# Kernel optimization log

Hardware: AMD Instinct MI355X
Metric: run time of the kernel (lower is better)

Reference implementation:

```python
import jax, jax.numpy as jnp
import numpy as np

N, D, B = 500000, 256, 2048

def setup_inputs() -> dict:
    key = jax.random.key(0)
    k1, k2, k3 = jax.random.split(key, 3)
    x = jax.random.normal(k1, (N, D), dtype=jnp.float32)
    batch_id = jnp.sort(jax.random.randint(k2, (N,), 0, B, dtype=jnp.int64))
    gate_w = jax.random.normal(k3, (D, 1), dtype=jnp.float32) * (1.0 / np.sqrt(D))
    gate_b = jnp.zeros((1,), dtype=jnp.float32)
    return {"x": x, "batch_id": batch_id, "batch_size": B, "gate_w": gate_w, "gate_b": gate_b}

def reference(x, batch_id, batch_size, gate_w, gate_b):
    # gate: Linear(D,1) + Sigmoid -> (N, 1)
    weights = jax.nn.sigmoid(x @ gate_w + gate_b)  # (N, 1)
    weighted = x * weights                          # (N, D)
    # scatter_add by graph id -> (B, D)
    pooled = jax.ops.segment_sum(weighted, batch_id, num_segments=batch_size)
    return pooled
```

## Files before the change

### kernel.cpp

```cpp
#include <hip/hip_runtime.h>

#define D_DIM 256
#define NWAVES 8192

typedef float v4f __attribute__((ext_vector_type(4)));

__device__ __forceinline__ float dot4(v4f v, v4f w) {
    return v[0]*w[0] + v[1]*w[1] + v[2]*w[2] + v[3]*w[3];
}
__device__ __forceinline__ float sigmoidf_(float t) {
    return 1.0f / (1.0f + __expf(-t));
}
__device__ __forceinline__ v4f vzero() {
    v4f z = {0.f, 0.f, 0.f, 0.f};
    return z;
}
__device__ __forceinline__ void flush_acc(float* __restrict__ out, int b,
                                          int lane, v4f acc) {
    float* p = out + (size_t)b * D_DIM + lane * 4;
    unsafeAtomicAdd(p + 0, acc[0]);
    unsafeAtomicAdd(p + 1, acc[1]);
    unsafeAtomicAdd(p + 2, acc[2]);
    unsafeAtomicAdd(p + 3, acc[3]);
}

__global__ __launch_bounds__(256) void attentive_readout_kernel(
    const float* __restrict__ x,
    const int* __restrict__ bid,
    const float* __restrict__ gw,
    const float* __restrict__ gb,
    float* __restrict__ out,
    int n)
{
    int gtid = blockIdx.x * blockDim.x + threadIdx.x;
    int wave = gtid >> 6;
    int lane = threadIdx.x & 63;

    const int base = n / NWAVES, rem = n % NWAVES;
    long long r0 = (long long)wave * base + (wave < rem ? wave : rem);
    long long r1 = r0 + base + (wave < rem ? 1 : 0);

    const v4f w4 = *(const v4f*)(gw + lane * 4);
    const float bias = gb[0];

    v4f acc = vzero();
    int cur = bid[r0];

    const float* px = x + (size_t)r0 * D_DIM + lane * 4;
    long long r = r0;
    const int nfull = (int)((r1 - r0) >> 2);

    v4f c0, c1, c2, c3;
    int cb0, cb1, cb2, cb3;
    if (nfull > 0) {
        c0 = __builtin_nontemporal_load((const v4f*)(px + 0 * D_DIM));
        c1 = __builtin_nontemporal_load((const v4f*)(px + 1 * D_DIM));
        c2 = __builtin_nontemporal_load((const v4f*)(px + 2 * D_DIM));
        c3 = __builtin_nontemporal_load((const v4f*)(px + 3 * D_DIM));
        cb0 = bid[r + 0]; cb1 = bid[r + 1]; cb2 = bid[r + 2]; cb3 = bid[r + 3];
    }

    for (int it = 0; it < nfull; ++it) {
        v4f n0, n1, n2, n3;
        int nb0 = 0, nb1 = 0, nb2 = 0, nb3 = 0;
        const float* pn = px + 4 * D_DIM;
        const bool more = (it + 1 < nfull);
        if (more) {
            n0 = __builtin_nontemporal_load((const v4f*)(pn + 0 * D_DIM));
            n1 = __builtin_nontemporal_load((const v4f*)(pn + 1 * D_DIM));
            n2 = __builtin_nontemporal_load((const v4f*)(pn + 2 * D_DIM));
            n3 = __builtin_nontemporal_load((const v4f*)(pn + 3 * D_DIM));
            nb0 = bid[r + 4]; nb1 = bid[r + 5]; nb2 = bid[r + 6]; nb3 = bid[r + 7];
        } else {
            n0 = c0; n1 = c1; n2 = c2; n3 = c3;
        }

        float s0 = dot4(c0, w4);
        float s1 = dot4(c1, w4);
        float s2 = dot4(c2, w4);
        float s3 = dot4(c3, w4);
        #pragma unroll
        for (int off = 32; off > 0; off >>= 1) {
            s0 += __shfl_xor(s0, off, 64);
            s1 += __shfl_xor(s1, off, 64);
            s2 += __shfl_xor(s2, off, 64);
            s3 += __shfl_xor(s3, off, 64);
        }
        float g0 = sigmoidf_(s0 + bias);
        float g1 = sigmoidf_(s1 + bias);
        float g2 = sigmoidf_(s2 + bias);
        float g3 = sigmoidf_(s3 + bias);

        if ((cb0 == cur) & (cb1 == cur) & (cb2 == cur) & (cb3 == cur)) {
            acc += c0 * g0 + c1 * g1 + c2 * g2 + c3 * g3;
        } else {
            if (cb0 != cur) { flush_acc(out, cur, lane, acc); acc = vzero(); cur = cb0; }
            acc += c0 * g0;
            if (cb1 != cur) { flush_acc(out, cur, lane, acc); acc = vzero(); cur = cb1; }
            acc += c1 * g1;
            if (cb2 != cur) { flush_acc(out, cur, lane, acc); acc = vzero(); cur = cb2; }
            acc += c2 * g2;
            if (cb3 != cur) { flush_acc(out, cur, lane, acc); acc = vzero(); cur = cb3; }
            acc += c3 * g3;
        }

        c0 = n0; c1 = n1; c2 = n2; c3 = n3;
        cb0 = nb0; cb1 = nb1; cb2 = nb2; cb3 = nb3;
        px = pn; r += 4;
    }

    for (; r < r1; ++r) {
        v4f v = __builtin_nontemporal_load((const v4f*)px);
        px += D_DIM;
        float s = dot4(v, w4);
        #pragma unroll
        for (int off = 32; off > 0; off >>= 1)
            s += __shfl_xor(s, off, 64);
        float g = sigmoidf_(s + bias);
        int b = bid[r];
        if (b != cur) { flush_acc(out, cur, lane, acc); acc = vzero(); cur = b; }
        acc += v * g;
    }
    flush_acc(out, cur, lane, acc);
}

extern "C" void kernel_launch(void* const* d_in, const int* in_sizes, int n_in,
                              void* d_out, int out_size, void* d_ws, size_t ws_size,
                              hipStream_t stream) {
    const float* x   = (const float*)d_in[0];
    const int*   bid = (const int*)d_in[1];
    const float* gw  = (const float*)d_in[3];
    const float* gb  = (const float*)d_in[4];
    float*       out = (float*)d_out;

    const int n = in_sizes[0] / D_DIM;

    hipMemsetAsync(d_out, 0, (size_t)out_size * sizeof(float), stream);

    const int threads = 256;
    const int blocks  = NWAVES / 4;

    attentive_readout_kernel<<<blocks, threads, 0, stream>>>(
        x, bid, gw, gb, out, n);
}
```

Baseline: 106.7 us.

## Double-buffer row groups per wave and use fixed 64-row wave chunks

The streaming loop now keeps two 4-row groups in flight in a ping-pong register scheme, so 8 rows of loads are outstanding while one group is reduced and accumulated. The work split changes from 8192 waves with uneven row ranges to fixed aligned 64-row chunks per wave, which lets the batch ids be fetched with a single int4 load. The aim is more memory-level parallelism on a bandwidth-bound stream. The cost is more live vector registers, which can lower occupancy.

```diff
diff --git a/kernel.cpp b/kernel.cpp
--- a/kernel.cpp
+++ b/kernel.cpp
@@ -1,7 +1,7 @@
 #include <hip/hip_runtime.h>
 
 #define D_DIM 256
-#define NWAVES 8192
+#define RPW   64
 
 typedef float v4f __attribute__((ext_vector_type(4)));
 
@@ -24,6 +24,53 @@
     unsafeAtomicAdd(p + 3, acc[3]);
 }
 
+__device__ __forceinline__ void prefetch_group(v4f& c0, v4f& c1, v4f& c2, v4f& c3,
+                                               int4& cb,
+                                               const float* px, const int* pb,
+                                               bool pred) {
+    if (pred) {
+        c0 = __builtin_nontemporal_load((const v4f*)(px + 0 * D_DIM));
+        c1 = __builtin_nontemporal_load((const v4f*)(px + 1 * D_DIM));
+        c2 = __builtin_nontemporal_load((const v4f*)(px + 2 * D_DIM));
+        c3 = __builtin_nontemporal_load((const v4f*)(px + 3 * D_DIM));
+        cb = *(const int4*)pb;
+    }
+}
+
+__device__ __forceinline__ void process_group(v4f c0, v4f c1, v4f c2, v4f c3,
+                                              int4 cb, v4f w4, float bias,
+                                              v4f& acc, int& cur,
+                                              float* __restrict__ out, int lane) {
+    float s0 = dot4(c0, w4);
+    float s1 = dot4(c1, w4);
+    float s2 = dot4(c2, w4);
+    float s3 = dot4(c3, w4);
+    #pragma unroll
+    for (int off = 32; off > 0; off >>= 1) {
+        s0 += __shfl_xor(s0, off, 64);
+        s1 += __shfl_xor(s1, off, 64);
+        s2 += __shfl_xor(s2, off, 64);
+        s3 += __shfl_xor(s3, off, 64);
+    }
+    float g0 = sigmoidf_(s0 + bias);
+    float g1 = sigmoidf_(s1 + bias);
+    float g2 = sigmoidf_(s2 + bias);
+    float g3 = sigmoidf_(s3 + bias);
+
+    if ((cb.x == cur) & (cb.y == cur) & (cb.z == cur) & (cb.w == cur)) {
+        acc += c0 * g0 + c1 * g1 + c2 * g2 + c3 * g3;
+    } else {
+        if (cb.x != cur) { flush_acc(out, cur, lane, acc); acc = vzero(); cur = cb.x; }
+        acc += c0 * g0;
+        if (cb.y != cur) { flush_acc(out, cur, lane, acc); acc = vzero(); cur = cb.y; }
+        acc += c1 * g1;
+        if (cb.z != cur) { flush_acc(out, cur, lane, acc); acc = vzero(); cur = cb.z; }
+        acc += c2 * g2;
+        if (cb.w != cur) { flush_acc(out, cur, lane, acc); acc = vzero(); cur = cb.w; }
+        acc += c3 * g3;
+    }
+}
+
 __global__ __launch_bounds__(256) void attentive_readout_kernel(
     const float* __restrict__ x,
     const int* __restrict__ bid,
@@ -36,9 +83,11 @@
     int wave = gtid >> 6;
     int lane = threadIdx.x & 63;
 
-    const int base = n / NWAVES, rem = n % NWAVES;
-    long long r0 = (long long)wave * base + (wave < rem ? wave : rem);
-    long long r1 = r0 + base + (wave < rem ? 1 : 0);
+    long long r0 = (long long)wave * RPW;
+    if (r0 >= n) return;
+    long long r1 = r0 + RPW;
+    if (r1 > n) r1 = n;
+    const int ngroups = (int)((r1 - r0) >> 2);
 
     const v4f w4 = *(const v4f*)(gw + lane * 4);
     const float bias = gb[0];
@@ -46,69 +95,34 @@
     v4f acc = vzero();
     int cur = bid[r0];
 
-    const float* px = x + (size_t)r0 * D_DIM + lane * 4;
-    long long r = r0;
-    const int nfull = (int)((r1 - r0) >> 2);
+    const float* pxa = x + (size_t)r0 * D_DIM + lane * 4;
+    const float* pxb = pxa + 4 * D_DIM;
+    const int*   pba = bid + r0;
+    const int*   pbb = pba + 4;
 
-    v4f c0, c1, c2, c3;
-    int cb0, cb1, cb2, cb3;
-    if (nfull > 0) {
-        c0 = __builtin_nontemporal_load((const v4f*)(px + 0 * D_DIM));
-        c1 = __builtin_nontemporal_load((const v4f*)(px + 1 * D_DIM));
-        c2 = __builtin_nontemporal_load((const v4f*)(px + 2 * D_DIM));
-        c3 = __builtin_nontemporal_load((const v4f*)(px + 3 * D_DIM));
-        cb0 = bid[r + 0]; cb1 = bid[r + 1]; cb2 = bid[r + 2]; cb3 = bid[r + 3];
+    v4f a0, a1, a2, a3, b0, b1, b2, b3;
+    int4 ab, bb;
+    prefetch_group(a0, a1, a2, a3, ab, pxa, pba, ngroups > 0);
+    prefetch_group(b0, b1, b2, b3, bb, pxb, pbb, ngroups > 1);
+
+    int g = 0;
+    for (; g + 2 <= ngroups; g += 2) {
+        process_group(a0, a1, a2, a3, ab, w4, bias, acc, cur, out, lane);
+        prefetch_group(a0, a1, a2, a3, ab, pxa + 8 * D_DIM, pba + 8,
+                       g + 2 < ngroups);
+        pxa += 8 * D_DIM; pba += 8;
+
+        process_group(b0, b1, b2, b3, bb, w4, bias, acc, cur, out, lane);
+        prefetch_group(b0, b1, b2, b3, bb, pxb + 8 * D_DIM, pbb + 8,
+                       g + 3 < ngroups);
+        pxb += 8 * D_DIM; pbb += 8;
+    }
+    if (g < ngroups) {
+        process_group(a0, a1, a2, a3, ab, w4, bias, acc, cur, out, lane);
     }
 
-    for (int it = 0; it < nfull; ++it) {
-        v4f n0, n1, n2, n3;
-        int nb0 = 0, nb1 = 0, nb2 = 0, nb3 = 0;
-        const float* pn = px + 4 * D_DIM;
-        const bool more = (it + 1 < nfull);
-        if (more) {
-            n0 = __builtin_nontemporal_load((const v4f*)(pn + 0 * D_DIM));
-            n1 = __builtin_nontemporal_load((const v4f*)(pn + 1 * D_DIM));
-            n2 = __builtin_nontemporal_load((const v4f*)(pn + 2 * D_DIM));
-            n3 = __builtin_nontemporal_load((const v4f*)(pn + 3 * D_DIM));
-            nb0 = bid[r + 4]; nb1 = bid[r + 5]; nb2 = bid[r + 6]; nb3 = bid[r + 7];
-        } else {
-            n0 = c0; n1 = c1; n2 = c2; n3 = c3;
-        }
-
-        float s0 = dot4(c0, w4);
-        float s1 = dot4(c1, w4);
-        float s2 = dot4(c2, w4);
-        float s3 = dot4(c3, w4);
-        #pragma unroll
-        for (int off = 32; off > 0; off >>= 1) {
-            s0 += __shfl_xor(s0, off, 64);
-            s1 += __shfl_xor(s1, off, 64);
-            s2 += __shfl_xor(s2, off, 64);
-            s3 += __shfl_xor(s3, off, 64);
-        }
-        float g0 = sigmoidf_(s0 + bias);
-        float g1 = sigmoidf_(s1 + bias);
-        float g2 = sigmoidf_(s2 + bias);
-        float g3 = sigmoidf_(s3 + bias);
-
-        if ((cb0 == cur) & (cb1 == cur) & (cb2 == cur) & (cb3 == cur)) {
-            acc += c0 * g0 + c1 * g1 + c2 * g2 + c3 * g3;
-        } else {
-            if (cb0 != cur) { flush_acc(out, cur, lane, acc); acc = vzero(); cur = cb0; }
-            acc += c0 * g0;
-            if (cb1 != cur) { flush_acc(out, cur, lane, acc); acc = vzero(); cur = cb1; }
-            acc += c1 * g1;
-            if (cb2 != cur) { flush_acc(out, cur, lane, acc); acc = vzero(); cur = cb2; }
-            acc += c2 * g2;
-            if (cb3 != cur) { flush_acc(out, cur, lane, acc); acc = vzero(); cur = cb3; }
-            acc += c3 * g3;
-        }
-
-        c0 = n0; c1 = n1; c2 = n2; c3 = n3;
-        cb0 = nb0; cb1 = nb1; cb2 = nb2; cb3 = nb3;
-        px = pn; r += 4;
-    }
-
+    long long r = r0 + ((long long)ngroups << 2);
+    const float* px = x + (size_t)r * D_DIM + lane * 4;
     for (; r < r1; ++r) {
         v4f v = __builtin_nontemporal_load((const v4f*)px);
         px += D_DIM;
@@ -116,10 +130,10 @@
         #pragma unroll
         for (int off = 32; off > 0; off >>= 1)
             s += __shfl_xor(s, off, 64);
-        float g = sigmoidf_(s + bias);
+        float gg = sigmoidf_(s + bias);
         int b = bid[r];
         if (b != cur) { flush_acc(out, cur, lane, acc); acc = vzero(); cur = b; }
-        acc += v * g;
+        acc += v * gg;
     }
     flush_acc(out, cur, lane, acc);
 }
@@ -138,7 +152,8 @@
     hipMemsetAsync(d_out, 0, (size_t)out_size * sizeof(float), stream);
 
     const int threads = 256;
-    const int blocks  = NWAVES / 4;
+    const int waves   = (n + RPW - 1) / RPW;
+    const int blocks  = (waves + 3) / 4;
 
     attentive_readout_kernel<<<blocks, threads, 0, stream>>>(
         x, bid, gw, gb, out, n);
```

Measured after the change: 104.5 us. 2.1% less time.
